# Kernel optimization log

Measured on AMD Instinct MI355X. Metric: run time of the kernel, lower is better.

## Reference

```python
import jax, jax.numpy as jnp
import numpy as np

NUM_HEADS = 16
HIDDEN = 1024
HEAD_DIM = HIDDEN // NUM_HEADS


def setup_inputs() -> dict:
    key = jax.random.key(0)
    ks = jax.random.split(key, 9)
    B, S, D = 2, 2048, HIDDEN
    s = 1.0 / np.sqrt(D)
    return {
        "x": jax.random.normal(ks[0], (B, S, D), dtype=jnp.float32),
        "Wq": jax.random.normal(ks[1], (D, D), dtype=jnp.float32) * s,
        "bq": jnp.zeros((D,), dtype=jnp.float32),
        "Wk": jax.random.normal(ks[2], (D, D), dtype=jnp.float32) * s,
        "bk": jnp.zeros((D,), dtype=jnp.float32),
        "Wv": jax.random.normal(ks[3], (D, D), dtype=jnp.float32) * s,
        "bv": jnp.zeros((D,), dtype=jnp.float32),
        "Wo": jax.random.normal(ks[4], (D, D), dtype=jnp.float32) * s,
        "bo": jnp.zeros((D,), dtype=jnp.float32),
    }


def reference(x, Wq, bq, Wk, bk, Wv, bv, Wo, bo):
    B, S, D = x.shape
    H, Hd = NUM_HEADS, HEAD_DIM
    # projections -> [B, H, S, Hd]
    def proj(W, b):
        return (x @ W + b).reshape(B, S, H, Hd).transpose(0, 2, 1, 3)
    q = proj(Wq, bq)
    k = proj(Wk, bk)
    v = proj(Wv, bv)
    scores = jnp.einsum('bhqd,bhkd->bhqk', q, k) / jnp.sqrt(jnp.float32(Hd))
    p_attn = jax.nn.softmax(scores, axis=-1)  # dropout = identity (eval)
    ctx = jnp.einsum('bhqk,bhkd->bhqd', p_attn, v)
    attn_mean = jnp.mean(p_attn, axis=1)  # [B, S, S]
    out = ctx.transpose(0, 2, 1, 3).reshape(B, S, D) @ Wo + bo
    return out, attn_mean
```

## Files before the change

kernel.cpp:

```cpp
#include <hip/hip_runtime.h>
#include <math.h>

#define NUM_HEADS 16
#define HEAD_DIM  64
#define HIDDEN    1024
#define BATCH     2
#define SEQ       2048

#define QSCALE 0.1803368801111204f

typedef short bf16x8 __attribute__((ext_vector_type(8)));
typedef short short4v __attribute__((ext_vector_type(4)));
typedef float f32x4 __attribute__((ext_vector_type(4)));

#if __has_builtin(__builtin_amdgcn_exp2f)
#define EXP2F __builtin_amdgcn_exp2f
#else
#define EXP2F exp2f
#endif

#define ACQB(N) do { asm volatile("s_waitcnt vmcnt(" #N ")" ::: "memory"); \
                     __builtin_amdgcn_s_barrier(); } while (0)
#define RELB()  do { asm volatile("s_waitcnt lgkmcnt(0)" ::: "memory");   \
                     __builtin_amdgcn_sched_barrier(0);                    \
                     __builtin_amdgcn_s_barrier(); } while (0)

__device__ __forceinline__ short f2bf(float f) {
    union { float f; unsigned int u; } x; x.f = f;
    unsigned int r = x.u + 0x7fffu + ((x.u >> 16) & 1u);
    return (short)(r >> 16);
}

__device__ __forceinline__ unsigned int pack_bf16_trunc(float lo, float hi) {
    return __builtin_amdgcn_perm(__float_as_uint(hi), __float_as_uint(lo), 0x07060302u);
}

__device__ __forceinline__ void async16(const void* g, void* l) {
    __builtin_amdgcn_global_load_lds(
        (const __attribute__((address_space(1))) void*)g,
        (__attribute__((address_space(3))) void*)l, 16, 0, 0);
}

__global__ __launch_bounds__(256)
void prep_kernel(const float* __restrict__ x,
                 const float* __restrict__ Wq, const float* __restrict__ Wk,
                 const float* __restrict__ Wv, const float* __restrict__ Wo,
                 short* __restrict__ xb, short* __restrict__ Wt4)
{
    __shared__ float t[64][65];
    const int tid = threadIdx.x;
    const int bid = blockIdx.x;
    if (bid < 4096) {
        size_t i = ((size_t)bid * 256 + tid) * 4;
        float4 v = *(const float4*)&x[i];
        short4v o;
        o.x = f2bf(v.x); o.y = f2bf(v.y); o.z = f2bf(v.z); o.w = f2bf(v.w);
        *(short4v*)&xb[i] = o;
        return;
    }
    const int tb = bid - 4096;
    const int z  = tb >> 8;
    const int cx = tb & 15, cy = (tb >> 4) & 15;
    const float* W = (z == 0) ? Wq : (z == 1) ? Wk : (z == 2) ? Wv : Wo;
    short* dst = Wt4 + (size_t)z * HIDDEN * HIDDEN;
    const int c0 = cx * 64;
    const int r0 = cy * 64;
    const int cl = tid & 63, rw = tid >> 6;
    #pragma unroll
    for (int p = 0; p < 16; ++p) {
        int row = p * 4 + rw;
        t[row][cl] = W[(size_t)(r0 + row) * HIDDEN + c0 + cl];
    }
    __syncthreads();
    #pragma unroll
    for (int p = 0; p < 16; ++p) {
        int orow = p * 4 + rw;
        dst[(size_t)(c0 + orow) * HIDDEN + r0 + cl] = f2bf(t[cl][orow]);
    }
}

__global__ __launch_bounds__(256)
void qkv_proj_kernel(const short* __restrict__ xb, const short* __restrict__ Wt4,
                     const float* __restrict__ bq, const float* __restrict__ bk,
                     const float* __restrict__ bv,
                     short* __restrict__ Qb, short* __restrict__ Kb,
                     short* __restrict__ Vt)
{
    __shared__ short ldsA[128 * 64];
    __shared__ short ldsB[128 * 64];
    const int tid = threadIdx.x;
    const int lane = tid & 63, w = tid >> 6;
    const int l = lane & 15, q = lane >> 4;
    const int lin = blockIdx.y * 8 + blockIdx.x;
    const int cid = (lin & 7) * 32 + (lin >> 3);
    const int n0 = (cid & 7) * 128;
    const int m0 = (cid >> 3) * 128;
    const int z  = blockIdx.z;
    const short* Wt = Wt4 + (size_t)z * HIDDEN * HIDDEN;
    const int wm = (w >> 1) * 64, wn = (w & 1) * 64;
    const int sw = l & 7;

    const short* pa[4]; const short* pb[4]; int ldst[4];
    #pragma unroll
    for (int hh = 0; hh < 4; ++hh) {
        int c = hh * 256 + tid;
        int row = c >> 3;
        int kcg = (c & 7) ^ (row & 7);
        pa[hh] = xb + (size_t)(m0 + row) * HIDDEN + kcg * 8;
        pb[hh] = Wt + (size_t)(n0 + row) * HIDDEN + kcg * 8;
        ldst[hh] = c * 8;
    }

    f32x4 acc[4][4];
    #pragma unroll
    for (int i = 0; i < 4; ++i)
        #pragma unroll
        for (int j = 0; j < 4; ++j)
            acc[i][j] = (f32x4){0.f, 0.f, 0.f, 0.f};

    auto STG = [&]() {
        #pragma unroll
        for (int hh = 0; hh < 4; ++hh) {
            async16(pa[hh], &ldsA[ldst[hh]]);
            async16(pb[hh], &ldsB[ldst[hh]]);
            pa[hh] += 64; pb[hh] += 64;
        }
    };

    STG();
    ACQB(0);
    for (int t = 0; t < 16; ++t) {
        bf16x8 af[4][2], bfr[4][2];
        #pragma unroll
        for (int kk = 0; kk < 2; ++kk) {
            const int cc = ((4 * kk + q) ^ sw) * 8;
            #pragma unroll
            for (int i = 0; i < 4; ++i)
                af[i][kk] = *(const bf16x8*)&ldsA[(wm + 16 * i + l) * 64 + cc];
            #pragma unroll
            for (int j = 0; j < 4; ++j)
                bfr[j][kk] = *(const bf16x8*)&ldsB[(wn + 16 * j + l) * 64 + cc];
        }
        RELB();
        if (t < 15) STG();
        __builtin_amdgcn_s_setprio(1);
        #pragma unroll
        for (int kk = 0; kk < 2; ++kk)
            #pragma unroll
            for (int i = 0; i < 4; ++i)
                #pragma unroll
                for (int j = 0; j < 4; ++j)
                    acc[i][j] = __builtin_amdgcn_mfma_f32_16x16x32_bf16(
                        af[i][kk], bfr[j][kk], acc[i][j], 0, 0, 0);
        __builtin_amdgcn_s_setprio(0);
        if (t < 15) ACQB(0);
    }

    const float* bias = (z == 0) ? bq : (z == 1) ? bk : bv;
    const float sc = (z == 0) ? QSCALE : 1.0f;
    if (z < 2) {
        short* Ob = (z == 0) ? Qb : Kb;
        #pragma unroll
        for (int j = 0; j < 4; ++j) {
            int n = n0 + wn + 16 * j + l;
            float bval = bias[n];
            int h = n >> 6, hd = n & 63;
            #pragma unroll
            for (int i = 0; i < 4; ++i) {
                #pragma unroll
                for (int reg = 0; reg < 4; ++reg) {
                    int m = m0 + wm + 16 * i + 4 * q + reg;
                    int b_ = m >> 11, s = m & 2047;
                    Ob[(((size_t)(b_ * NUM_HEADS + h) * SEQ) + s) * HEAD_DIM + hd] =
                        f2bf((acc[i][j][reg] + bval) * sc);
                }
            }
        }
    } else {
        #pragma unroll
        for (int j = 0; j < 4; ++j) {
            int n = n0 + wn + 16 * j + l;
            float bval = bias[n];
            int h = n >> 6, hd = n & 63;
            #pragma unroll
            for (int i = 0; i < 4; ++i) {
                int mb = m0 + wm + 16 * i + 4 * q;
                int b_ = mb >> 11, s = mb & 2047;
                short4v pk;
                #pragma unroll
                for (int reg = 0; reg < 4; ++reg)
                    pk[reg] = f2bf(acc[i][j][reg] + bval);
                *(short4v*)&Vt[(((size_t)(b_ * NUM_HEADS + h) * HEAD_DIM) + hd) * SEQ + s] = pk;
            }
        }
    }
}

__global__ __launch_bounds__(512, 4)
void flash_kernel(const short* __restrict__ Qb, const short* __restrict__ Kb,
                  const short* __restrict__ Vt, short* __restrict__ Cb,
                  float* __restrict__ Lb)
{
    __shared__ __align__(16) char fsm[35840];
    short (*Ks)[64 * 64] = (short (*)[64 * 64])fsm;
    short (*Vs)[64 * 64] = (short (*)[64 * 64])(fsm + 16384);
    float (*Xch)[64][35] = (float (*)[64][35])fsm;

    const int tid = threadIdx.x, lane = tid & 63, w = tid >> 6;
    const int l = lane & 15, q = lane >> 4;
    const int qg = w & 3;
    const int kh = w >> 2;
    const int q0 = blockIdx.x * 128;
    const int Q0 = q0 + qg * 32;
    const int h = blockIdx.y, b = blockIdx.z;
    const size_t base  = (size_t)(b * NUM_HEADS + h) * SEQ * HEAD_DIM;
    const size_t vbase = (size_t)(b * NUM_HEADS + h) * HEAD_DIM * SEQ;

    bf16x8 bq[2][2];
    #pragma unroll
    for (int u = 0; u < 2; ++u)
        #pragma unroll
        for (int ks = 0; ks < 2; ++ks)
            bq[u][ks] = *(const bf16x8*)(Qb + base +
                (size_t)(Q0 + 16 * u + l) * HEAD_DIM + 32 * ks + 8 * q);

    const int c = tid;
    const int row = c >> 3;
    const int g = ((c & 7) ^ (row & 7)) * 8;
    const short* kp = Kb + base + (size_t)row * HEAD_DIM + g;
    const short* vp = Vt + vbase + (size_t)row * SEQ + g;

    const int sw = l & 15 & 7;
    int kaddr[2];
    #pragma unroll
    for (int ks = 0; ks < 2; ++ks)
        kaddr[ks] = (32 * kh + l) * 64 + ((4 * ks + q) ^ sw) * 8;
    const int vc0 = 4 * kh + (q >> 1);
    const int vaddr0 = l * 64 + ((vc0      ^ sw) * 8) + 4 * (q & 1);
    const int vaddr1 = l * 64 + (((vc0 + 2) ^ sw) * 8) + 4 * (q & 1);

    f32x4 ctx[2][4];
    #pragma unroll
    for (int u = 0; u < 2; ++u)
        #pragma unroll
        for (int m = 0; m < 4; ++m) ctx[u][m] = (f32x4){0.f, 0.f, 0.f, 0.f};
    float l_part[2] = {0.f, 0.f};

    auto STG = [&](int buf) {
        async16(kp, &Ks[buf][c * 8]);
        async16(vp, &Vs[buf][c * 8]);
        kp += 64 * HEAD_DIM;
        vp += 64;
    };
    auto CMP = [&](int buf) {
        f32x4 st[2][2];
        #pragma unroll
        for (int u = 0; u < 2; ++u)
            #pragma unroll
            for (int t = 0; t < 2; ++t) st[u][t] = (f32x4){0.f, 0.f, 0.f, 0.f};
        __builtin_amdgcn_s_setprio(1);
        #pragma unroll
        for (int ks = 0; ks < 2; ++ks) {
            #pragma unroll
            for (int t = 0; t < 2; ++t) {
                bf16x8 ak = *(const bf16x8*)&Ks[buf][kaddr[ks] + t * 1024];
                st[0][t] = __builtin_amdgcn_mfma_f32_16x16x32_bf16(ak, bq[0][ks], st[0][t], 0, 0, 0);
                st[1][t] = __builtin_amdgcn_mfma_f32_16x16x32_bf16(ak, bq[1][ks], st[1][t], 0, 0, 0);
            }
        }
        __builtin_amdgcn_s_setprio(0);
        union { unsigned int u32[4]; bf16x8 v; } bp[2];
        #pragma unroll
        for (int u = 0; u < 2; ++u) {
            #pragma unroll
            for (int t = 0; t < 2; ++t) {
                float p0 = EXP2F(st[u][t][0]);
                float p1 = EXP2F(st[u][t][1]);
                float p2 = EXP2F(st[u][t][2]);
                float p3 = EXP2F(st[u][t][3]);
                l_part[u] += (p0 + p1) + (p2 + p3);
                bp[u].u32[2 * t]     = pack_bf16_trunc(p0, p1);
                bp[u].u32[2 * t + 1] = pack_bf16_trunc(p2, p3);
            }
        }
        __builtin_amdgcn_s_setprio(1);
        #pragma unroll
        for (int m = 0; m < 4; ++m) {
            short4v g0 = *(const short4v*)&Vs[buf][vaddr0 + m * 1024];
            short4v g1 = *(const short4v*)&Vs[buf][vaddr1 + m * 1024];
            bf16x8 av = __builtin_shufflevector(g0, g1, 0, 1, 2, 3, 4, 5, 6, 7);
            ctx[0][m] = __builtin_amdgcn_mfma_f32_16x16x32_bf16(av, bp[0].v, ctx[0][m], 0, 0, 0);
            ctx[1][m] = __builtin_amdgcn_mfma_f32_16x16x32_bf16(av, bp[1].v, ctx[1][m], 0, 0, 0);
        }
        __builtin_amdgcn_s_setprio(0);
    };

    STG(0); STG(1);
    ACQB(2);
    for (int tp = 0; tp < 15; ++tp) {
        CMP(0); RELB(); STG(0); ACQB(2);
        CMP(1); RELB(); STG(1); ACQB(2);
    }
    CMP(0); RELB(); ACQB(0);
    CMP(1);

    __syncthreads();

    if (kh == 1) {
        float* dst = &Xch[qg][lane][0];
        #pragma unroll
        for (int u = 0; u < 2; ++u)
            #pragma unroll
            for (int m = 0; m < 4; ++m)
                #pragma unroll
                for (int r = 0; r < 4; ++r)
                    dst[u * 16 + m * 4 + r] = ctx[u][m][r];
        dst[32] = l_part[0];
        dst[33] = l_part[1];
    }
    __syncthreads();
    if (kh == 0) {
        const float* src = &Xch[qg][lane][0];
        #pragma unroll
        for (int u = 0; u < 2; ++u)
            #pragma unroll
            for (int m = 0; m < 4; ++m)
                #pragma unroll
                for (int r = 0; r < 4; ++r)
                    ctx[u][m][r] += src[u * 16 + m * 4 + r];

        #pragma unroll
        for (int u = 0; u < 2; ++u) {
            float rs = l_part[u] + src[32 + u];
            rs += __shfl_xor(rs, 16);
            rs += __shfl_xor(rs, 32);
            float inv_l = 1.0f / rs;
            int s = Q0 + 16 * u + l;
            #pragma unroll
            for (int t = 0; t < 4; ++t) {
                short4v pk;
                #pragma unroll
                for (int reg = 0; reg < 4; ++reg)
                    pk[reg] = f2bf(ctx[u][t][reg] * inv_l);
                *(short4v*)&Cb[(((size_t)(b * NUM_HEADS + h) * SEQ) + s) * HEAD_DIM + 16 * t + 4 * q] = pk;
            }
            if (q == 0)
                Lb[(size_t)(b * NUM_HEADS + h) * SEQ + s] = inv_l;
        }
    }
}

__global__ __launch_bounds__(256)
void tail_kernel(const short* __restrict__ Cb, const short* __restrict__ Wot,
                 const float* __restrict__ bo, float* __restrict__ out,
                 const short* __restrict__ Qb, const short* __restrict__ Kb,
                 const float* __restrict__ Lb, float* __restrict__ amean)
{
    __shared__ __align__(16) short smem[26624];
    const int tid = threadIdx.x, lane = tid & 63, w = tid >> 6;
    const int l = lane & 15, q = lane >> 4;
    const int sw = l & 7;
    const int bid = blockIdx.x;
    const int r3 = bid % 3, g3 = bid / 3;

    if (r3 == 2) {
        short (*ldsA)[64 * 64]  = (short (*)[64 * 64])smem;
        short (*ldsB)[128 * 64] = (short (*)[128 * 64])(smem + 8192);
        const int cid = (g3 & 7) * 64 + (g3 >> 3);
        const int n0 = (cid & 7) * 128;
        const int m0 = (cid >> 3) * 64;

        const short* pa[2]; const short* pb[4]; int lda[2], ldb[4];
        #pragma unroll
        for (int hh = 0; hh < 2; ++hh) {
            int cc = hh * 256 + tid;
            int rowc = cc >> 3;
            int kcg = (cc & 7) ^ (rowc & 7);
            int m = m0 + rowc;
            int b_ = m >> 11, s = m & 2047;
            pa[hh] = Cb + (((size_t)(b_ * NUM_HEADS) * SEQ) + s) * HEAD_DIM + kcg * 8;
            lda[hh] = cc * 8;
        }
        #pragma unroll
        for (int hh = 0; hh < 4; ++hh) {
            int cc = hh * 256 + tid;
            int rowc = cc >> 3;
            int kcg = (cc & 7) ^ (rowc & 7);
            pb[hh] = Wot + (size_t)(n0 + rowc) * HIDDEN + kcg * 8;
            ldb[hh] = cc * 8;
        }

        f32x4 acc[4][2];
        #pragma unroll
        for (int i = 0; i < 4; ++i)
            #pragma unroll
            for (int jj = 0; jj < 2; ++jj)
                acc[i][jj] = (f32x4){0.f, 0.f, 0.f, 0.f};

        auto STG = [&](int buf) {
            #pragma unroll
            for (int hh = 0; hh < 2; ++hh) {
                async16(pa[hh], &ldsA[buf][lda[hh]]);
                pa[hh] += (size_t)SEQ * HEAD_DIM;
            }
            #pragma unroll
            for (int hh = 0; hh < 4; ++hh) {
                async16(pb[hh], &ldsB[buf][ldb[hh]]);
                pb[hh] += 64;
            }
        };
        auto CMP = [&](int buf) {
            #pragma unroll
            for (int kk = 0; kk < 2; ++kk) {
                const int cc = ((4 * kk + q) ^ sw) * 8;
                bf16x8 af[4], bfr[2];
                #pragma unroll
                for (int i = 0; i < 4; ++i)
                    af[i] = *(const bf16x8*)&ldsA[buf][(16 * i + l) * 64 + cc];
                #pragma unroll
                for (int jj = 0; jj < 2; ++jj)
                    bfr[jj] = *(const bf16x8*)&ldsB[buf][(32 * w + 16 * jj + l) * 64 + cc];
                __builtin_amdgcn_s_setprio(1);
                #pragma unroll
                for (int i = 0; i < 4; ++i)
                    #pragma unroll
                    for (int jj = 0; jj < 2; ++jj)
                        acc[i][jj] = __builtin_amdgcn_mfma_f32_16x16x32_bf16(
                            af[i], bfr[jj], acc[i][jj], 0, 0, 0);
                __builtin_amdgcn_s_setprio(0);
            }
        };

        STG(0);
        for (int t = 0; t < 15; ++t) {
            STG((t & 1) ^ 1);
            ACQB(6);
            CMP(t & 1);
            RELB();
        }
        ACQB(0);
        CMP(1);

        #pragma unroll
        for (int jj = 0; jj < 2; ++jj) {
            int n = n0 + 32 * w + 16 * jj + l;
            float bval = bo[n];
            #pragma unroll
            for (int i = 0; i < 4; ++i)
                #pragma unroll
                for (int reg = 0; reg < 4; ++reg) {
                    int m = m0 + 16 * i + 4 * q + reg;
                    out[(size_t)m * HIDDEN + n] = acc[i][jj][reg] + bval;
                }
        }
    } else {
        short (*Qs)[64 * 64]  = (short (*)[64 * 64])smem;
        short (*Ks)[128 * 64] = (short (*)[128 * 64])(smem + 8192);
        float* Ls = (float*)(smem + 24576);
        const int a  = g3 * 2 + r3;
        const int k0 = (a & 15) * 128;
        const int qy = (a >> 4) & 31;
        const int q0 = qy * 64;
        const int b  = a >> 9;
        const size_t HSTRIDE = (size_t)SEQ * HEAD_DIM;

        const short* qp[2];
        const short* kp[4];
        {
            const size_t base0 = (size_t)(b * NUM_HEADS) * HSTRIDE;
            #pragma unroll
            for (int i = 0; i < 2; ++i) {
                int cc = 256 * i + tid;
                int rowc = cc >> 3;
                int gg = ((cc & 7) ^ (rowc & 7)) * 8;
                qp[i] = Qb + base0 + (size_t)(q0 + rowc) * HEAD_DIM + gg;
            }
            #pragma unroll
            for (int i = 0; i < 4; ++i) {
                int cc = 256 * i + tid;
                int rowc = cc >> 3;
                int gg = ((cc & 7) ^ (rowc & 7)) * 8;
                kp[i] = Kb + base0 + (size_t)(k0 + rowc) * HEAD_DIM + gg;
            }
        }

        f32x4 macc[2][4];
        #pragma unroll
        for (int tk = 0; tk < 2; ++tk)
            #pragma unroll
            for (int tq = 0; tq < 4; ++tq)
                macc[tk][tq] = (f32x4){0.f, 0.f, 0.f, 0.f};

        auto STG = [&](int buf) {
            #pragma unroll
            for (int i = 0; i < 2; ++i) { async16(qp[i], &Qs[buf][(256 * i + tid) * 8]); qp[i] += HSTRIDE; }
            #pragma unroll
            for (int i = 0; i < 4; ++i) { async16(kp[i], &Ks[buf][(256 * i + tid) * 8]); kp[i] += HSTRIDE; }
        };
        int hc = 0;
        auto CMP = [&](int buf) {
            int h = hc++;
            float linv[4];
            #pragma unroll
            for (int tq = 0; tq < 4; ++tq)
                linv[tq] = Ls[h * 64 + 16 * tq + l];

            bf16x8 bq[4][2], ak[2][2];
            #pragma unroll
            for (int ks = 0; ks < 2; ++ks) {
                const int cc = ((4 * ks + q) ^ sw) * 8;
                #pragma unroll
                for (int tq = 0; tq < 4; ++tq)
                    bq[tq][ks] = *(const bf16x8*)&Qs[buf][(16 * tq + l) * 64 + cc];
                #pragma unroll
                for (int tk = 0; tk < 2; ++tk)
                    ak[tk][ks] = *(const bf16x8*)&Ks[buf][(32 * w + 16 * tk + l) * 64 + cc];
            }
            #pragma unroll
            for (int tk = 0; tk < 2; ++tk) {
                #pragma unroll
                for (int tq = 0; tq < 4; ++tq) {
                    f32x4 st = (f32x4){0.f, 0.f, 0.f, 0.f};
                    st = __builtin_amdgcn_mfma_f32_16x16x32_bf16(ak[tk][0], bq[tq][0], st, 0, 0, 0);
                    st = __builtin_amdgcn_mfma_f32_16x16x32_bf16(ak[tk][1], bq[tq][1], st, 0, 0, 0);
                    float li = linv[tq];
                    #pragma unroll
                    for (int reg = 0; reg < 4; ++reg)
                        macc[tk][tq][reg] += EXP2F(st[reg]) * li;
                }
            }
        };

        {
            int hh = tid >> 4, cc = tid & 15;
            async16(Lb + ((size_t)(b * NUM_HEADS) + hh) * SEQ + q0 + cc * 4,
                    &Ls[hh * 64 + cc * 4]);
        }
        STG(0); STG(1);
        ACQB(6);
        for (int tp = 0; tp < 7; ++tp) {
            CMP(0); RELB(); STG(0); ACQB(6);
            CMP(1); RELB(); STG(1); ACQB(6);
        }
        CMP(0); RELB(); ACQB(0);
        CMP(1);

        const float inv_h = 1.0f / (float)NUM_HEADS;
        #pragma unroll
        for (int tq = 0; tq < 4; ++tq) {
            int row_q = q0 + 16 * tq + l;
            #pragma unroll
            for (int tk = 0; tk < 2; ++tk) {
                int col_k = k0 + 32 * w + 16 * tk + 4 * q;
                f32x4 o;
                #pragma unroll
                for (int reg = 0; reg < 4; ++reg) o[reg] = macc[tk][tq][reg] * inv_h;
                *(f32x4*)&amean[((size_t)b * SEQ + row_q) * SEQ + col_k] = o;
            }
        }
    }
}

extern "C" void kernel_launch(void* const* d_in, const int* in_sizes, int n_in,
                              void* d_out, int out_size, void* d_ws, size_t ws_size,
                              hipStream_t stream)
{
    const float* x  = (const float*)d_in[0];
    const float* Wq = (const float*)d_in[1];
    const float* bq = (const float*)d_in[2];
    const float* Wk = (const float*)d_in[3];
    const float* bk = (const float*)d_in[4];
    const float* Wv = (const float*)d_in[5];
    const float* bv = (const float*)d_in[6];
    const float* Wo = (const float*)d_in[7];
    const float* bo = (const float*)d_in[8];

    float* out   = (float*)d_out;
    float* amean = out + (size_t)BATCH * SEQ * HIDDEN;

    const size_t NELEM = (size_t)BATCH * NUM_HEADS * SEQ * HEAD_DIM;
    short* ws  = (short*)d_ws;
    short* xb  = ws;
    short* Wt4 = xb + NELEM;
    short* Qb  = Wt4 + 4 * (size_t)HIDDEN * HIDDEN;
    short* Kb  = Qb + NELEM;
    short* Vt  = Kb + NELEM;
    short* Cb  = Vt + NELEM;
    float* Lb  = (float*)(Cb + NELEM);

    dim3 blk(256);
    prep_kernel<<<dim3(4096 + 1024), blk, 0, stream>>>(x, Wq, Wk, Wv, Wo, xb, Wt4);
    qkv_proj_kernel<<<dim3(8, 32, 3), blk, 0, stream>>>(xb, Wt4, bq, bk, bv, Qb, Kb, Vt);
    flash_kernel<<<dim3(SEQ / 128, NUM_HEADS, BATCH), dim3(512), 0, stream>>>(Qb, Kb, Vt, Cb, Lb);
    tail_kernel<<<dim3(1536), blk, 0, stream>>>(Cb, Wt4 + 3 * (size_t)HIDDEN * HIDDEN, bo, out,
                                                Qb, Kb, Lb, amean);
}
```

Baseline: 219.5 us.

## Enlarge tail kernel tiles to 128x128 with 2x2 wave layout

The tail kernel's output-projection GEMM and attention-mean recompute now use 128x128 tiles instead of 64x128, with waves arranged 2x2 so each wave computes a 64x64 sub-tile. Block count halves and LDS use grows to hold the larger Q/A tiles. The aim is to raise arithmetic intensity and cut redundant global/LDS loads per MFMA. In exchange each block needs more accumulator registers and more LDS, which can lower occupancy, and there are fewer blocks to spread across CUs.

```diff
diff --git a/kernel.cpp b/kernel.cpp
--- a/kernel.cpp
+++ b/kernel.cpp
@@ -230,7 +230,7 @@
     const short* kp = Kb + base + (size_t)row * HEAD_DIM + g;
     const short* vp = Vt + vbase + (size_t)row * SEQ + g;
 
-    const int sw = l & 15 & 7;
+    const int sw = l & 7;
     int kaddr[2];
     #pragma unroll
     for (int ks = 0; ks < 2; ++ks)
@@ -356,7 +356,7 @@
                  const short* __restrict__ Qb, const short* __restrict__ Kb,
                  const float* __restrict__ Lb, float* __restrict__ amean)
 {
-    __shared__ __align__(16) short smem[26624];
+    __shared__ __align__(16) short smem[36864];
     const int tid = threadIdx.x, lane = tid & 63, w = tid >> 6;
     const int l = lane & 15, q = lane >> 4;
     const int sw = l & 7;
@@ -364,48 +364,38 @@
     const int r3 = bid % 3, g3 = bid / 3;
 
     if (r3 == 2) {
-        short (*ldsA)[64 * 64]  = (short (*)[64 * 64])smem;
-        short (*ldsB)[128 * 64] = (short (*)[128 * 64])(smem + 8192);
-        const int cid = (g3 & 7) * 64 + (g3 >> 3);
-        const int n0 = (cid & 7) * 128;
-        const int m0 = (cid >> 3) * 64;
-
-        const short* pa[2]; const short* pb[4]; int lda[2], ldb[4];
-        #pragma unroll
-        for (int hh = 0; hh < 2; ++hh) {
+        short (*ldsA)[128 * 64] = (short (*)[128 * 64])smem;
+        short (*ldsB)[128 * 64] = (short (*)[128 * 64])(smem + 16384);
+        const int n0 = (g3 & 7) * 128;
+        const int m0 = (g3 >> 3) * 128;
+        const int wm = (w >> 1) * 64, wn = (w & 1) * 64;
+
+        const short* pa[4]; const short* pb[4]; int ldst[4];
+        #pragma unroll
+        for (int hh = 0; hh < 4; ++hh) {
             int cc = hh * 256 + tid;
             int rowc = cc >> 3;
             int kcg = (cc & 7) ^ (rowc & 7);
             int m = m0 + rowc;
             int b_ = m >> 11, s = m & 2047;
             pa[hh] = Cb + (((size_t)(b_ * NUM_HEADS) * SEQ) + s) * HEAD_DIM + kcg * 8;
-            lda[hh] = cc * 8;
-        }
-        #pragma unroll
-        for (int hh = 0; hh < 4; ++hh) {
-            int cc = hh * 256 + tid;
-            int rowc = cc >> 3;
-            int kcg = (cc & 7) ^ (rowc & 7);
             pb[hh] = Wot + (size_t)(n0 + rowc) * HIDDEN + kcg * 8;
-            ldb[hh] = cc * 8;
-        }
-
-        f32x4 acc[4][2];
+            ldst[hh] = cc * 8;
+        }
+
+        f32x4 acc[4][4];
         #pragma unroll
         for (int i = 0; i < 4; ++i)
             #pragma unroll
-            for (int jj = 0; jj < 2; ++jj)
-                acc[i][jj] = (f32x4){0.f, 0.f, 0.f, 0.f};
+            for (int j = 0; j < 4; ++j)
+                acc[i][j] = (f32x4){0.f, 0.f, 0.f, 0.f};
 
         auto STG = [&](int buf) {
             #pragma unroll
-            for (int hh = 0; hh < 2; ++hh) {
-                async16(pa[hh], &ldsA[buf][lda[hh]]);
+            for (int hh = 0; hh < 4; ++hh) {
+                async16(pa[hh], &ldsA[buf][ldst[hh]]);
+                async16(pb[hh], &ldsB[buf][ldst[hh]]);
                 pa[hh] += (size_t)SEQ * HEAD_DIM;
-            }
-            #pragma unroll
-            for (int hh = 0; hh < 4; ++hh) {
-                async16(pb[hh], &ldsB[buf][ldb[hh]]);
                 pb[hh] += 64;
             }
         };
@@ -413,20 +403,20 @@
             #pragma unroll
             for (int kk = 0; kk < 2; ++kk) {
                 const int cc = ((4 * kk + q) ^ sw) * 8;
-                bf16x8 af[4], bfr[2];
+                bf16x8 af[4], bfr[4];
                 #pragma unroll
                 for (int i = 0; i < 4; ++i)
-                    af[i] = *(const bf16x8*)&ldsA[buf][(16 * i + l) * 64 + cc];
-                #pragma unroll
-                for (int jj = 0; jj < 2; ++jj)
-                    bfr[jj] = *(const bf16x8*)&ldsB[buf][(32 * w + 16 * jj + l) * 64 + cc];
+                    af[i] = *(const bf16x8*)&ldsA[buf][(wm + 16 * i + l) * 64 + cc];
+                #pragma unroll
+                for (int j = 0; j < 4; ++j)
+                    bfr[j] = *(const bf16x8*)&ldsB[buf][(wn + 16 * j + l) * 64 + cc];
                 __builtin_amdgcn_s_setprio(1);
                 #pragma unroll
                 for (int i = 0; i < 4; ++i)
                     #pragma unroll
-                    for (int jj = 0; jj < 2; ++jj)
-                        acc[i][jj] = __builtin_amdgcn_mfma_f32_16x16x32_bf16(
-                            af[i], bfr[jj], acc[i][jj], 0, 0, 0);
+                    for (int j = 0; j < 4; ++j)
+                        acc[i][j] = __builtin_amdgcn_mfma_f32_16x16x32_bf16(
+                            af[i], bfr[j], acc[i][j], 0, 0, 0);
                 __builtin_amdgcn_s_setprio(0);
             }
         };
@@ -434,7 +424,7 @@
         STG(0);
         for (int t = 0; t < 15; ++t) {
             STG((t & 1) ^ 1);
-            ACQB(6);
+            ACQB(8);
             CMP(t & 1);
             RELB();
         }
@@ -442,60 +432,58 @@
         CMP(1);
 
         #pragma unroll
-        for (int jj = 0; jj < 2; ++jj) {
-            int n = n0 + 32 * w + 16 * jj + l;
+        for (int j = 0; j < 4; ++j) {
+            int n = n0 + wn + 16 * j + l;
             float bval = bo[n];
             #pragma unroll
             for (int i = 0; i < 4; ++i)
                 #pragma unroll
                 for (int reg = 0; reg < 4; ++reg) {
-                    int m = m0 + 16 * i + 4 * q + reg;
-                    out[(size_t)m * HIDDEN + n] = acc[i][jj][reg] + bval;
+                    int m = m0 + wm + 16 * i + 4 * q + reg;
+                    out[(size_t)m * HIDDEN + n] = acc[i][j][reg] + bval;
                 }
         }
     } else {
-        short (*Qs)[64 * 64]  = (short (*)[64 * 64])smem;
-        short (*Ks)[128 * 64] = (short (*)[128 * 64])(smem + 8192);
-        float* Ls = (float*)(smem + 24576);
+        short (*Qs)[128 * 64] = (short (*)[128 * 64])smem;
+        short (*Ks)[128 * 64] = (short (*)[128 * 64])(smem + 16384);
+        float* Ls = (float*)(smem + 32768);
         const int a  = g3 * 2 + r3;
         const int k0 = (a & 15) * 128;
-        const int qy = (a >> 4) & 31;
-        const int q0 = qy * 64;
-        const int b  = a >> 9;
+        const int q0 = ((a >> 4) & 15) * 128;
+        const int b  = a >> 8;
+        const int wk0 = (w & 1) * 64, wq0 = (w >> 1) * 64;
         const size_t HSTRIDE = (size_t)SEQ * HEAD_DIM;
 
-        const short* qp[2];
+        const short* qp[4];
         const short* kp[4];
+        int ldst[4];
         {
             const size_t base0 = (size_t)(b * NUM_HEADS) * HSTRIDE;
             #pragma unroll
-            for (int i = 0; i < 2; ++i) {
+            for (int i = 0; i < 4; ++i) {
                 int cc = 256 * i + tid;
                 int rowc = cc >> 3;
                 int gg = ((cc & 7) ^ (rowc & 7)) * 8;
                 qp[i] = Qb + base0 + (size_t)(q0 + rowc) * HEAD_DIM + gg;
-            }
-            #pragma unroll
-            for (int i = 0; i < 4; ++i) {
-                int cc = 256 * i + tid;
-                int rowc = cc >> 3;
-                int gg = ((cc & 7) ^ (rowc & 7)) * 8;
                 kp[i] = Kb + base0 + (size_t)(k0 + rowc) * HEAD_DIM + gg;
-            }
-        }
-
-        f32x4 macc[2][4];
-        #pragma unroll
-        for (int tk = 0; tk < 2; ++tk)
+                ldst[i] = cc * 8;
+            }
+        }
+
+        f32x4 macc[4][4];
+        #pragma unroll
+        for (int tk = 0; tk < 4; ++tk)
             #pragma unroll
             for (int tq = 0; tq < 4; ++tq)
                 macc[tk][tq] = (f32x4){0.f, 0.f, 0.f, 0.f};
 
         auto STG = [&](int buf) {
             #pragma unroll
-            for (int i = 0; i < 2; ++i) { async16(qp[i], &Qs[buf][(256 * i + tid) * 8]); qp[i] += HSTRIDE; }
-            #pragma unroll
-            for (int i = 0; i < 4; ++i) { async16(kp[i], &Ks[buf][(256 * i + tid) * 8]); kp[i] += HSTRIDE; }
+            for (int i = 0; i < 4; ++i) {
+                async16(qp[i], &Qs[buf][ldst[i]]);
+                async16(kp[i], &Ks[buf][ldst[i]]);
+                qp[i] += HSTRIDE; kp[i] += HSTRIDE;
+            }
         };
         int hc = 0;
         auto CMP = [&](int buf) {
@@ -503,21 +491,21 @@
             float linv[4];
             #pragma unroll
             for (int tq = 0; tq < 4; ++tq)
-                linv[tq] = Ls[h * 64 + 16 * tq + l];
-
-            bf16x8 bq[4][2], ak[2][2];
+                linv[tq] = Ls[h * 128 + wq0 + 16 * tq + l];
+
+            bf16x8 ak[4][2], bq[4][2];
             #pragma unroll
             for (int ks = 0; ks < 2; ++ks) {
                 const int cc = ((4 * ks + q) ^ sw) * 8;
                 #pragma unroll
+                for (int tk = 0; tk < 4; ++tk)
+                    ak[tk][ks] = *(const bf16x8*)&Ks[buf][(wk0 + 16 * tk + l) * 64 + cc];
+                #pragma unroll
                 for (int tq = 0; tq < 4; ++tq)
-                    bq[tq][ks] = *(const bf16x8*)&Qs[buf][(16 * tq + l) * 64 + cc];
-                #pragma unroll
-                for (int tk = 0; tk < 2; ++tk)
-                    ak[tk][ks] = *(const bf16x8*)&Ks[buf][(32 * w + 16 * tk + l) * 64 + cc];
-            }
-            #pragma unroll
-            for (int tk = 0; tk < 2; ++tk) {
+                    bq[tq][ks] = *(const bf16x8*)&Qs[buf][(wq0 + 16 * tq + l) * 64 + cc];
+            }
+            #pragma unroll
+            for (int tk = 0; tk < 4; ++tk) {
                 #pragma unroll
                 for (int tq = 0; tq < 4; ++tq) {
                     f32x4 st = (f32x4){0.f, 0.f, 0.f, 0.f};
@@ -532,15 +520,20 @@
         };
 
         {
-            int hh = tid >> 4, cc = tid & 15;
-            async16(Lb + ((size_t)(b * NUM_HEADS) + hh) * SEQ + q0 + cc * 4,
-                    &Ls[hh * 64 + cc * 4]);
+            #pragma unroll
+            for (int i = 0; i < 2; ++i) {
+                int cc = 256 * i + tid;
+                int hh = cc >> 5;
+                int off = (cc & 31) * 4;
+                async16(Lb + ((size_t)(b * NUM_HEADS) + hh) * SEQ + q0 + off,
+                        &Ls[hh * 128 + off]);
+            }
         }
         STG(0); STG(1);
-        ACQB(6);
+        ACQB(8);
         for (int tp = 0; tp < 7; ++tp) {
-            CMP(0); RELB(); STG(0); ACQB(6);
-            CMP(1); RELB(); STG(1); ACQB(6);
+            CMP(0); RELB(); STG(0); ACQB(8);
+            CMP(1); RELB(); STG(1); ACQB(8);
         }
         CMP(0); RELB(); ACQB(0);
         CMP(1);
@@ -548,10 +541,10 @@
         const float inv_h = 1.0f / (float)NUM_HEADS;
         #pragma unroll
         for (int tq = 0; tq < 4; ++tq) {
-            int row_q = q0 + 16 * tq + l;
-            #pragma unroll
-            for (int tk = 0; tk < 2; ++tk) {
-                int col_k = k0 + 32 * w + 16 * tk + 4 * q;
+            int row_q = q0 + wq0 + 16 * tq + l;
+            #pragma unroll
+            for (int tk = 0; tk < 4; ++tk) {
+                int col_k = k0 + wk0 + 16 * tk + 4 * q;
                 f32x4 o;
                 #pragma unroll
                 for (int reg = 0; reg < 4; ++reg) o[reg] = macc[tk][tq][reg] * inv_h;
@@ -592,6 +585,6 @@
     prep_kernel<<<dim3(4096 + 1024), blk, 0, stream>>>(x, Wq, Wk, Wv, Wo, xb, Wt4);
     qkv_proj_kernel<<<dim3(8, 32, 3), blk, 0, stream>>>(xb, Wt4, bq, bk, bv, Qb, Kb, Vt);
     flash_kernel<<<dim3(SEQ / 128, NUM_HEADS, BATCH), dim3(512), 0, stream>>>(Qb, Kb, Vt, Cb, Lb);
-    tail_kernel<<<dim3(1536), blk, 0, stream>>>(Cb, Wt4 + 3 * (size_t)HIDDEN * HIDDEN, bo, out,
-                                                Qb, Kb, Lb, amean);
-}
+    tail_kernel<<<dim3(768), blk, 0, stream>>>(Cb, Wt4 + 3 * (size_t)HIDDEN * HIDDEN, bo, out,
+                                               Qb, Kb, Lb, amean);
+}
```

Result: slower. 238.6 us (+8.7%).

## Use single-barrier double-buffer pipeline with full waits in all three phases

Applied to the files above, without the earlier changes.

Replaces the two-barrier acquire/release double-buffer loops in the attention, output-projection and attention-mean phases with a one-barrier-per-iteration scheme. Each iteration waits for all outstanding loads and LDS ops, then issues the next tile's async load into the other buffer, then computes on the current buffer. This halves the barrier count per tile. In exchange, each wait drains all in-flight global loads, so prefetch depth drops to a single tile and load latency may be hidden less. A redundant mask in the swizzle computation is also simplified.

```diff
diff --git a/kernel.cpp b/kernel.cpp
--- a/kernel.cpp
+++ b/kernel.cpp
@@ -22,6 +22,9 @@
 #define ACQB(N) do { asm volatile("s_waitcnt vmcnt(" #N ")" ::: "memory"); \
                      __builtin_amdgcn_s_barrier(); } while (0)
 #define RELB()  do { asm volatile("s_waitcnt lgkmcnt(0)" ::: "memory");   \
+                     __builtin_amdgcn_sched_barrier(0);                    \
+                     __builtin_amdgcn_s_barrier(); } while (0)
+#define BARR()  do { asm volatile("s_waitcnt vmcnt(0) lgkmcnt(0)" ::: "memory"); \
                      __builtin_amdgcn_sched_barrier(0);                    \
                      __builtin_amdgcn_s_barrier(); } while (0)
 
@@ -230,7 +233,7 @@
     const short* kp = Kb + base + (size_t)row * HEAD_DIM + g;
     const short* vp = Vt + vbase + (size_t)row * SEQ + g;
 
-    const int sw = l & 15 & 7;
+    const int sw = l & 7;
     int kaddr[2];
     #pragma unroll
     for (int ks = 0; ks < 2; ++ks)
@@ -295,14 +298,12 @@
         __builtin_amdgcn_s_setprio(0);
     };
 
-    STG(0); STG(1);
-    ACQB(2);
-    for (int tp = 0; tp < 15; ++tp) {
-        CMP(0); RELB(); STG(0); ACQB(2);
-        CMP(1); RELB(); STG(1); ACQB(2);
-    }
-    CMP(0); RELB(); ACQB(0);
-    CMP(1);
+    STG(0);
+    for (int t = 0; t < 32; ++t) {
+        BARR();
+        if (t < 31) STG((t + 1) & 1);
+        CMP(t & 1);
+    }
 
     __syncthreads();
 
@@ -432,14 +433,11 @@
         };
 
         STG(0);
-        for (int t = 0; t < 15; ++t) {
-            STG((t & 1) ^ 1);
-            ACQB(6);
+        for (int t = 0; t < 16; ++t) {
+            BARR();
+            if (t < 15) STG((t + 1) & 1);
             CMP(t & 1);
-            RELB();
-        }
-        ACQB(0);
-        CMP(1);
+        }
 
         #pragma unroll
         for (int jj = 0; jj < 2; ++jj) {
@@ -536,14 +534,12 @@
             async16(Lb + ((size_t)(b * NUM_HEADS) + hh) * SEQ + q0 + cc * 4,
                     &Ls[hh * 64 + cc * 4]);
         }
-        STG(0); STG(1);
-        ACQB(6);
-        for (int tp = 0; tp < 7; ++tp) {
-            CMP(0); RELB(); STG(0); ACQB(6);
-            CMP(1); RELB(); STG(1); ACQB(6);
-        }
-        CMP(0); RELB(); ACQB(0);
-        CMP(1);
+        STG(0);
+        for (int t = 0; t < 16; ++t) {
+            BARR();
+            if (t < 15) STG((t + 1) & 1);
+            CMP(t & 1);
+        }
 
         const float inv_h = 1.0f / (float)NUM_HEADS;
         #pragma unroll
```

New measurement: 218.5 us. About the same (-0.5%).
